# Kernel tuning notes

Hardware: AMD Instinct MI355X
Metric: run time of the kernel (lower is better)

The kernel has to match this reference:

```python
import jax, jax.numpy as jnp
import numpy as np

EPS = 1e-08
NEG_WEIGHT = 0.5
B, D = 4096, 256


def setup_inputs() -> dict:
    key = jax.random.key(0)
    k1, k2 = jax.random.split(key)
    feature_a = jax.random.normal(k1, (B, D), dtype=jnp.float32)
    feature_b = jax.random.normal(k2, (B, D), dtype=jnp.float32)
    labels = jnp.ones((B,), dtype=jnp.float32)  # positive pairs on the diagonal block
    return {"feature_a": feature_a, "feature_b": feature_b, "labels": labels}


def reference(feature_a, feature_b, labels):
    b = feature_a.shape[0]
    num_neg = b - 1
    # Cosine via single GEMM instead of the torch repeat/cat loop.
    # torch.nn.CosineSimilarity: dot / max(||a||*||b||, eps)
    na = jnp.sqrt(jnp.sum(feature_a * feature_a, axis=1))  # [B]
    nb = jnp.sqrt(jnp.sum(feature_b * feature_b, axis=1))  # [B]
    dots = jnp.einsum('kd,jd->kj', feature_a, feature_b)   # [B,B] dots[k,j]=a_k.b_j
    # torch ordering: block s (shift), row k pairs a_k with b_{(k+s) % B}
    k = jnp.arange(b)
    s = jnp.arange(b)
    idx = (k[None, :] + s[:, None]) % b                    # [S,K]
    cos = dots[k[None, :], idx] / jnp.maximum(na[None, :] * nb[idx], EPS)  # [S,K]
    logits = ((cos + 1.0) * 0.5).reshape(-1)               # flatten s-major (matches torch cat order)
    labels_full = jnp.concatenate(
        [labels.reshape(-1), jnp.zeros((num_neg * b,), dtype=labels.dtype)])
    weight = jnp.concatenate(
        [jnp.ones((b,), dtype=logits.dtype),
         jnp.full((num_neg * b,), NEG_WEIGHT, dtype=logits.dtype)])
    # BCELoss(weight, reduction='sum') with torch's log clamp at -100
    log_p = jnp.maximum(jnp.log(logits), -100.0)
    log_1mp = jnp.maximum(jnp.log1p(-logits), -100.0)
    loss = -jnp.sum(weight * (labels_full * log_p + (1.0 - labels_full) * log_1mp))
    return (logits, loss)
```

## Files before the change

### kernel.cpp

```cpp
#include <hip/hip_runtime.h>
#include <stdint.h>

#define NB 4096
#define ND 256

typedef __attribute__((ext_vector_type(8))) short short8;
typedef __attribute__((ext_vector_type(4))) float f32x4;

__device__ __forceinline__ unsigned short f2bf(float f) {
    unsigned int u = __float_as_uint(f);
    u += 0x7FFFu + ((u >> 16) & 1u);
    return (unsigned short)(u >> 16);
}

__device__ __forceinline__ void gload16(const void* g, void* lds_uniform) {
    __builtin_amdgcn_global_load_lds(
        (const __attribute__((address_space(1))) void*)(uintptr_t)g,
        (__attribute__((address_space(3))) void*)(unsigned int)(uintptr_t)lds_uniform,
        16, 0, 0);
}

__global__ void __launch_bounds__(256) prep_kernel(
    const float* __restrict__ A, const float* __restrict__ Bf,
    unsigned short* __restrict__ Abf, unsigned short* __restrict__ Bbf,
    float* __restrict__ lossws)
{
    if (blockIdx.x == 0 && threadIdx.x < 64) lossws[threadIdx.x << 5] = 0.0f;
    int gw   = (blockIdx.x * 256 + threadIdx.x) >> 6;
    int lane = threadIdx.x & 63;
    const float* src; unsigned short* dst; int row;
    if (gw < NB) { src = A;  dst = Abf; row = gw; }
    else         { src = Bf; dst = Bbf; row = gw - NB; }

    float4 v = reinterpret_cast<const float4*>(src + (size_t)row * ND)[lane];
    float ss = v.x * v.x + v.y * v.y + v.z * v.z + v.w * v.w;
    #pragma unroll
    for (int off = 1; off < 64; off <<= 1) ss += __shfl_xor(ss, off);
    float rn = 1.0f / sqrtf(fmaxf(ss, 1e-30f));

    ushort4 u;
    u.x = f2bf(v.x * rn); u.y = f2bf(v.y * rn);
    u.z = f2bf(v.z * rn); u.w = f2bf(v.w * rn);
    reinterpret_cast<ushort4*>(dst + (size_t)row * ND)[lane] = u;
}

__global__ void __launch_bounds__(256, 4) gemm_kernel(
    const unsigned short* __restrict__ Abf, const unsigned short* __restrict__ Bbf,
    const float* __restrict__ labels, float* __restrict__ out,
    float* __restrict__ lossws)
{
    __shared__ __align__(16) char smem[40960];

    const int tid = threadIdx.x;
    const int w = tid >> 6, lane = tid & 63;
    const int lane15 = lane & 15, lhi = lane >> 4;
    const int bk = blockIdx.x & 31, bs = blockIdx.x >> 5;
    const int k0 = bk << 7, s0 = bs << 6;
    const int j0 = (k0 + s0) & (NB - 1);

    f32x4 acc[2][5];
    #pragma unroll
    for (int m = 0; m < 2; ++m)
        #pragma unroll
        for (int r = 0; r < 5; ++r) acc[m][r] = (f32x4)0.0f;

    const unsigned short* asrc[2];
    const unsigned short* bsrc[3];
    int aslot0[2], bslot0[3];
    #pragma unroll
    for (int i = 0; i < 2; ++i) {
        int slot0 = (i << 8) + (w << 6);
        int slot  = slot0 + lane;
        int row   = slot >> 2;
        int sch   = (slot ^ (slot >> 2) ^ (slot >> 4)) & 3;
        asrc[i]   = Abf + (size_t)(k0 + row) * ND + (sch << 3);
        aslot0[i] = slot0;
    }
    #pragma unroll
    for (int i = 0; i < 3; ++i) {
        int slot0 = (i << 8) + (w << 6);
        int slot  = slot0 + lane;
        int row   = slot >> 2;
        int srow  = (j0 + row) & (NB - 1);
        int sch   = (slot ^ (slot >> 2) ^ (slot >> 4)) & 3;
        bsrc[i]   = Bbf + (size_t)srow * ND + (sch << 3);
        bslot0[i] = slot0;
    }

    auto stage = [&](int kt, char* buf) {
        #pragma unroll
        for (int i = 0; i < 2; ++i)
            gload16(asrc[i] + (kt << 5), buf + aslot0[i] * 16);
        #pragma unroll
        for (int i = 0; i < 3; ++i)
            gload16(bsrc[i] + (kt << 5), buf + 8192 + bslot0[i] * 16);
    };

    stage(0, smem);
    __syncthreads();

    #pragma unroll
    for (int kt = 0; kt < 8; ++kt) {
        char* buf = smem + ((kt & 1) ? 20480 : 0);
        if (kt < 7) stage(kt + 1, smem + ((kt & 1) ? 0 : 20480));

        const int f = (lane15 ^ (lane15 >> 2)) & 3;
        short8 a[2], b[6];
        #pragma unroll
        for (int m = 0; m < 2; ++m) {
            int row = (w << 5) + (m << 4) + lane15;
            a[m] = *reinterpret_cast<const short8*>(buf + row * 64 + ((lhi ^ f) << 4));
        }
        #pragma unroll
        for (int jf = 0; jf < 6; ++jf) {
            int row = (w << 5) + (jf << 4) + lane15;
            b[jf] = *reinterpret_cast<const short8*>(buf + 8192 + row * 64 + ((lhi ^ f) << 4));
        }
        #pragma unroll
        for (int m = 0; m < 2; ++m)
            #pragma unroll
            for (int r = 0; r < 5; ++r)
                acc[m][r] = __builtin_amdgcn_mfma_f32_16x16x32_bf16(
                    a[m], b[m + r], acc[m][r], 0, 0, 0);
        __syncthreads();
    }

    float* dw    = reinterpret_cast<float*>(smem);
    float* lpart = reinterpret_cast<float*>(smem + 32768);
    #pragma unroll
    for (int m = 0; m < 2; ++m)
        #pragma unroll
        for (int r = 0; r < 5; ++r)
            #pragma unroll
            for (int e = 0; e < 4; ++e) {
                int t = (r << 4) + lane15 - (lhi << 2) - e;
                if ((unsigned)t < 64u) {
                    int kap = (w << 5) + (m << 4) + (lhi << 2) + e;
                    dw[(t << 7) + (kap ^ (t & 31))] = acc[m][r][e];
                }
            }
    __syncthreads();

    const int t = w + (lane15 << 2);
    const int s = s0 + t;
    const int x3 = w & 3;
    const float* rowp = dw + (t << 7);
    float lacc = 0.0f;

    #pragma unroll
    for (int i = 0; i < 8; ++i) {
        int qlog  = lhi + (i << 2);
        int physq = qlog ^ (lane15 & 7);
        f32x4 d = *reinterpret_cast<const f32x4*>(rowp + (physq << 2));
        f32x4 v;
        if      (x3 == 0) { v = d; }
        else if (x3 == 1) { v[0] = d[1]; v[1] = d[0]; v[2] = d[3]; v[3] = d[2]; }
        else if (x3 == 2) { v[0] = d[2]; v[1] = d[3]; v[2] = d[0]; v[3] = d[1]; }
        else              { v[0] = d[3]; v[1] = d[2]; v[2] = d[1]; v[3] = d[0]; }

        f32x4 x, y;
        #pragma unroll
        for (int e = 0; e < 4; ++e) {
            x[e] = fmaf(v[e],  0.5f, 0.5f);
            y[e] = fmaf(v[e], -0.5f, 0.5f);
        }
        *reinterpret_cast<f32x4*>(out + (size_t)s * NB + k0 + (qlog << 2)) = x;

        float l1p0 = fmaxf(__logf(y[0]), -100.0f);
        float l1p1 = fmaxf(__logf(y[1]), -100.0f);
        float l1p2 = fmaxf(__logf(y[2]), -100.0f);
        float l1p3 = fmaxf(__logf(y[3]), -100.0f);
        if (s == 0) {
            float l1pv[4] = {l1p0, l1p1, l1p2, l1p3};
            #pragma unroll
            for (int e = 0; e < 4; ++e) {
                float lab = labels[k0 + (qlog << 2) + e];
                float lp  = fmaxf(__logf(x[e]), -100.0f);
                lacc += lab * lp + (1.0f - lab) * l1pv[e];
            }
        } else {
            lacc += 0.5f * (l1p0 + l1p1 + l1p2 + l1p3);
        }
    }

    #pragma unroll
    for (int off = 32; off > 0; off >>= 1) lacc += __shfl_down(lacc, off);
    if (lane == 0) lpart[w] = lacc;
    __syncthreads();
    if (tid == 0) {
        float tot = lpart[0] + lpart[1] + lpart[2] + lpart[3];
        atomicAdd(lossws + ((blockIdx.x & 63) << 5), -tot);
    }
}

__global__ void finalize_kernel(const float* __restrict__ lossws, float* __restrict__ out) {
    float s = 0.0f;
    for (int i = 0; i < 64; ++i) s += lossws[i << 5];
    out[(size_t)NB * NB] = s;
}

extern "C" void kernel_launch(void* const* d_in, const int* in_sizes, int n_in,
                              void* d_out, int out_size, void* d_ws, size_t ws_size,
                              hipStream_t stream) {
    (void)in_sizes; (void)n_in; (void)out_size; (void)ws_size;
    const float* A      = (const float*)d_in[0];
    const float* Bf     = (const float*)d_in[1];
    const float* labels = (const float*)d_in[2];
    float* out = (float*)d_out;

    char* ws = (char*)d_ws;
    unsigned short* Abf = (unsigned short*)ws;
    unsigned short* Bbf = (unsigned short*)(ws + (size_t)2 * 1024 * 1024);
    float* lossws = (float*)(ws + (size_t)4 * 1024 * 1024);

    hipLaunchKernelGGL(prep_kernel, dim3(2048), dim3(256), 0, stream,
                       A, Bf, Abf, Bbf, lossws);
    hipLaunchKernelGGL(gemm_kernel, dim3(2048), dim3(256), 0, stream,
                       Abf, Bbf, labels, out, lossws);
    hipLaunchKernelGGL(finalize_kernel, dim3(1), dim3(1), 0, stream, lossws, out);
}
```

Measured before the change: 47.84 us.

## Enlarge GEMM tile to 128 shifts per block with 2x2 warp split

Each block now covers 128 k rows by 128 shifts instead of 128 by 64, and the four warps are split two along k and two along the shift. The B band is shared across both shift halves and each warp accumulates a 4x5 MFMA tile, so fewer redundant B loads are issued per output. The epilogue runs in two phases through the same LDS staging area. The grid is halved and the block index mapping is reordered. In exchange, LDS and register use rise, occupancy hint drops from 4 to 3 blocks, and an extra pair of barriers is added.

```diff
diff --git a/kernel.cpp b/kernel.cpp
--- a/kernel.cpp
+++ b/kernel.cpp
@@ -44,44 +44,44 @@
     reinterpret_cast<ushort4*>(dst + (size_t)row * ND)[lane] = u;
 }
 
-__global__ void __launch_bounds__(256, 4) gemm_kernel(
+__global__ void __launch_bounds__(256, 3) gemm_kernel(
     const unsigned short* __restrict__ Abf, const unsigned short* __restrict__ Bbf,
     const float* __restrict__ labels, float* __restrict__ out,
     float* __restrict__ lossws)
 {
-    __shared__ __align__(16) char smem[40960];
+    __shared__ __align__(16) char smem[49168];
 
     const int tid = threadIdx.x;
     const int w = tid >> 6, lane = tid & 63;
     const int lane15 = lane & 15, lhi = lane >> 4;
-    const int bk = blockIdx.x & 31, bs = blockIdx.x >> 5;
-    const int k0 = bk << 7, s0 = bs << 6;
+    const int kw_ = w >> 1, sw_ = w & 1;
+    const int bid = blockIdx.x;
+    const int bk = bid >> 5, bs = bid & 31;
+    const int k0 = bk << 7, s0 = bs << 7;
     const int j0 = (k0 + s0) & (NB - 1);
 
-    f32x4 acc[2][5];
-    #pragma unroll
-    for (int m = 0; m < 2; ++m)
-        #pragma unroll
-        for (int r = 0; r < 5; ++r) acc[m][r] = (f32x4)0.0f;
+    f32x4 acc[4][5];
+    #pragma unroll
+    for (int mk = 0; mk < 4; ++mk)
+        #pragma unroll
+        for (int r = 0; r < 5; ++r) acc[mk][r] = (f32x4)0.0f;
 
     const unsigned short* asrc[2];
-    const unsigned short* bsrc[3];
-    int aslot0[2], bslot0[3];
+    const unsigned short* bsrc[4];
+    int aslot0[2], bslot0[4];
     #pragma unroll
     for (int i = 0; i < 2; ++i) {
         int slot0 = (i << 8) + (w << 6);
         int slot  = slot0 + lane;
-        int row   = slot >> 2;
         int sch   = (slot ^ (slot >> 2) ^ (slot >> 4)) & 3;
-        asrc[i]   = Abf + (size_t)(k0 + row) * ND + (sch << 3);
+        asrc[i]   = Abf + (size_t)(k0 + (slot >> 2)) * ND + (sch << 3);
         aslot0[i] = slot0;
     }
     #pragma unroll
-    for (int i = 0; i < 3; ++i) {
+    for (int i = 0; i < 4; ++i) {
         int slot0 = (i << 8) + (w << 6);
         int slot  = slot0 + lane;
-        int row   = slot >> 2;
-        int srow  = (j0 + row) & (NB - 1);
+        int srow  = (j0 + (slot >> 2)) & (NB - 1);
         int sch   = (slot ^ (slot >> 2) ^ (slot >> 4)) & 3;
         bsrc[i]   = Bbf + (size_t)srow * ND + (sch << 3);
         bslot0[i] = slot0;
@@ -92,7 +92,7 @@
         for (int i = 0; i < 2; ++i)
             gload16(asrc[i] + (kt << 5), buf + aslot0[i] * 16);
         #pragma unroll
-        for (int i = 0; i < 3; ++i)
+        for (int i = 0; i < 4; ++i)
             gload16(bsrc[i] + (kt << 5), buf + 8192 + bslot0[i] * 16);
     };
 
@@ -101,86 +101,93 @@
 
     #pragma unroll
     for (int kt = 0; kt < 8; ++kt) {
-        char* buf = smem + ((kt & 1) ? 20480 : 0);
-        if (kt < 7) stage(kt + 1, smem + ((kt & 1) ? 0 : 20480));
+        char* buf = smem + ((kt & 1) ? 24576 : 0);
+        if (kt < 7) stage(kt + 1, smem + ((kt & 1) ? 0 : 24576));
 
         const int f = (lane15 ^ (lane15 >> 2)) & 3;
-        short8 a[2], b[6];
-        #pragma unroll
-        for (int m = 0; m < 2; ++m) {
-            int row = (w << 5) + (m << 4) + lane15;
-            a[m] = *reinterpret_cast<const short8*>(buf + row * 64 + ((lhi ^ f) << 4));
-        }
-        #pragma unroll
-        for (int jf = 0; jf < 6; ++jf) {
-            int row = (w << 5) + (jf << 4) + lane15;
-            b[jf] = *reinterpret_cast<const short8*>(buf + 8192 + row * 64 + ((lhi ^ f) << 4));
-        }
-        #pragma unroll
-        for (int m = 0; m < 2; ++m)
+        short8 a[4], b[8];
+        #pragma unroll
+        for (int mk = 0; mk < 4; ++mk) {
+            int row = (kw_ << 6) + (mk << 4) + lane15;
+            a[mk] = *reinterpret_cast<const short8*>(buf + row * 64 + ((lhi ^ f) << 4));
+        }
+        #pragma unroll
+        for (int q = 0; q < 8; ++q) {
+            int row = ((kw_ + sw_) << 6) + (q << 4) + lane15;
+            b[q] = *reinterpret_cast<const short8*>(buf + 8192 + row * 64 + ((lhi ^ f) << 4));
+        }
+        #pragma unroll
+        for (int mk = 0; mk < 4; ++mk)
             #pragma unroll
             for (int r = 0; r < 5; ++r)
-                acc[m][r] = __builtin_amdgcn_mfma_f32_16x16x32_bf16(
-                    a[m], b[m + r], acc[m][r], 0, 0, 0);
+                acc[mk][r] = __builtin_amdgcn_mfma_f32_16x16x32_bf16(
+                    a[mk], b[mk + r], acc[mk][r], 0, 0, 0);
         __syncthreads();
     }
 
     float* dw    = reinterpret_cast<float*>(smem);
-    float* lpart = reinterpret_cast<float*>(smem + 32768);
-    #pragma unroll
-    for (int m = 0; m < 2; ++m)
-        #pragma unroll
-        for (int r = 0; r < 5; ++r)
+    float* lpart = reinterpret_cast<float*>(smem + 49152);
+    float lacc = 0.0f;
+
+    #pragma unroll
+    for (int p = 0; p < 2; ++p) {
+        if (sw_ == p) {
+            #pragma unroll
+            for (int mk = 0; mk < 4; ++mk)
+                #pragma unroll
+                for (int r = 0; r < 5; ++r)
+                    #pragma unroll
+                    for (int e = 0; e < 4; ++e) {
+                        int t = (r << 4) + lane15 - (lhi << 2) - e;
+                        if ((unsigned)t < 64u) {
+                            int kap = (kw_ << 6) + (mk << 4) + (lhi << 2) + e;
+                            dw[(t << 7) + (kap ^ (t & 31))] = acc[mk][r][e];
+                        }
+                    }
+        }
+        __syncthreads();
+
+        const int t = w + (lane15 << 2);
+        const int s = s0 + (p << 6) + t;
+        const int x3 = w & 3;
+        const float* rowp = dw + (t << 7);
+
+        #pragma unroll
+        for (int i = 0; i < 8; ++i) {
+            int qlog  = lhi + (i << 2);
+            int physq = qlog ^ (lane15 & 7);
+            f32x4 d = *reinterpret_cast<const f32x4*>(rowp + (physq << 2));
+            f32x4 v;
+            if      (x3 == 0) { v = d; }
+            else if (x3 == 1) { v[0] = d[1]; v[1] = d[0]; v[2] = d[3]; v[3] = d[2]; }
+            else if (x3 == 2) { v[0] = d[2]; v[1] = d[3]; v[2] = d[0]; v[3] = d[1]; }
+            else              { v[0] = d[3]; v[1] = d[2]; v[2] = d[1]; v[3] = d[0]; }
+
+            f32x4 x, y;
             #pragma unroll
             for (int e = 0; e < 4; ++e) {
-                int t = (r << 4) + lane15 - (lhi << 2) - e;
-                if ((unsigned)t < 64u) {
-                    int kap = (w << 5) + (m << 4) + (lhi << 2) + e;
-                    dw[(t << 7) + (kap ^ (t & 31))] = acc[m][r][e];
+                x[e] = fmaf(v[e],  0.5f, 0.5f);
+                y[e] = fmaf(v[e], -0.5f, 0.5f);
+            }
+            *reinterpret_cast<f32x4*>(out + (size_t)s * NB + k0 + (qlog << 2)) = x;
+
+            float l1p0 = fmaxf(__logf(y[0]), -100.0f);
+            float l1p1 = fmaxf(__logf(y[1]), -100.0f);
+            float l1p2 = fmaxf(__logf(y[2]), -100.0f);
+            float l1p3 = fmaxf(__logf(y[3]), -100.0f);
+            if (s == 0) {
+                float l1pv[4] = {l1p0, l1p1, l1p2, l1p3};
+                #pragma unroll
+                for (int e = 0; e < 4; ++e) {
+                    float lab = labels[k0 + (qlog << 2) + e];
+                    float lp  = fmaxf(__logf(x[e]), -100.0f);
+                    lacc += lab * lp + (1.0f - lab) * l1pv[e];
                 }
+            } else {
+                lacc += 0.5f * (l1p0 + l1p1 + l1p2 + l1p3);
             }
-    __syncthreads();
-
-    const int t = w + (lane15 << 2);
-    const int s = s0 + t;
-    const int x3 = w & 3;
-    const float* rowp = dw + (t << 7);
-    float lacc = 0.0f;
-
-    #pragma unroll
-    for (int i = 0; i < 8; ++i) {
-        int qlog  = lhi + (i << 2);
-        int physq = qlog ^ (lane15 & 7);
-        f32x4 d = *reinterpret_cast<const f32x4*>(rowp + (physq << 2));
-        f32x4 v;
-        if      (x3 == 0) { v = d; }
-        else if (x3 == 1) { v[0] = d[1]; v[1] = d[0]; v[2] = d[3]; v[3] = d[2]; }
-        else if (x3 == 2) { v[0] = d[2]; v[1] = d[3]; v[2] = d[0]; v[3] = d[1]; }
-        else              { v[0] = d[3]; v[1] = d[2]; v[2] = d[1]; v[3] = d[0]; }
-
-        f32x4 x, y;
-        #pragma unroll
-        for (int e = 0; e < 4; ++e) {
-            x[e] = fmaf(v[e],  0.5f, 0.5f);
-            y[e] = fmaf(v[e], -0.5f, 0.5f);
-        }
-        *reinterpret_cast<f32x4*>(out + (size_t)s * NB + k0 + (qlog << 2)) = x;
-
-        float l1p0 = fmaxf(__logf(y[0]), -100.0f);
-        float l1p1 = fmaxf(__logf(y[1]), -100.0f);
-        float l1p2 = fmaxf(__logf(y[2]), -100.0f);
-        float l1p3 = fmaxf(__logf(y[3]), -100.0f);
-        if (s == 0) {
-            float l1pv[4] = {l1p0, l1p1, l1p2, l1p3};
-            #pragma unroll
-            for (int e = 0; e < 4; ++e) {
-                float lab = labels[k0 + (qlog << 2) + e];
-                float lp  = fmaxf(__logf(x[e]), -100.0f);
-                lacc += lab * lp + (1.0f - lab) * l1pv[e];
-            }
-        } else {
-            lacc += 0.5f * (l1p0 + l1p1 + l1p2 + l1p3);
-        }
+        }
+        __syncthreads();
     }
 
     #pragma unroll
@@ -189,7 +196,7 @@
     __syncthreads();
     if (tid == 0) {
         float tot = lpart[0] + lpart[1] + lpart[2] + lpart[3];
-        atomicAdd(lossws + ((blockIdx.x & 63) << 5), -tot);
+        atomicAdd(lossws + ((bid & 63) << 5), -tot);
     }
 }
 
@@ -215,7 +222,7 @@
 
     hipLaunchKernelGGL(prep_kernel, dim3(2048), dim3(256), 0, stream,
                        A, Bf, Abf, Bbf, lossws);
-    hipLaunchKernelGGL(gemm_kernel, dim3(2048), dim3(256), 0, stream,
+    hipLaunchKernelGGL(gemm_kernel, dim3(1024), dim3(256), 0, stream,
                        Abf, Bbf, labels, out, lossws);
     hipLaunchKernelGGL(finalize_kernel, dim3(1), dim3(1), 0, stream, lossws, out);
 }
```

Measured after the change: 50.18 us. +4.9%, slower.
